# Kernel optimization log

Measured on AMD Instinct MI355X. Metric: run time of the kernel, lower is better.

The kernel has to match this reference:

```python
import jax, jax.numpy as jnp
import numpy as np

SEQ_LEN = 4096
HIDDEN = 1280
NUM_HEADS = 16
HEAD_DIM = HIDDEN // NUM_HEADS  # 80
NUM_SEQS = 8


def setup_inputs() -> dict:
    key = jax.random.key(0)
    ks = jax.random.split(key, 8)
    x = jax.random.normal(ks[0], (SEQ_LEN, HIDDEN), dtype=jnp.float32)
    # rotary tables: use cos/sin of random angles so they are bounded like real RoPE tables
    ang = jax.random.uniform(ks[1], (SEQ_LEN, HEAD_DIM), dtype=jnp.float32) * 6.283185
    cos = jnp.cos(ang)
    sin = jnp.sin(ang)
    # variable-length packed segments: strictly increasing boundaries incl. 0 and SEQ_LEN
    rng = np.random.default_rng(0)
    inner = np.sort(rng.choice(np.arange(1, SEQ_LEN), size=NUM_SEQS - 1, replace=False))
    cu_seqlens = jnp.asarray(np.concatenate([[0], inner, [SEQ_LEN]]), dtype=jnp.int32)
    s = 0.02
    w_qkv = jax.random.normal(ks[2], (HIDDEN, 3 * HIDDEN), dtype=jnp.float32) * s
    b_qkv = jnp.zeros((3 * HIDDEN,), dtype=jnp.float32)
    w_proj = jax.random.normal(ks[3], (HIDDEN, HIDDEN), dtype=jnp.float32) * s
    b_proj = jnp.zeros((HIDDEN,), dtype=jnp.float32)
    return {"x": x, "cu_seqlens": cu_seqlens, "cos": cos, "sin": sin,
            "w_qkv": w_qkv, "b_qkv": b_qkv, "w_proj": w_proj, "b_proj": b_proj}


def _rotate_half(t):
    d = t.shape[-1] // 2
    return jnp.concatenate([-t[..., d:], t[..., :d]], axis=-1)


def _apply_rope(q, k, cos, sin):
    # q,k: (S,H,D); cos,sin: (S,D) broadcast over heads, computed in fp32
    c = cos[:, None, :].astype(jnp.float32)
    s = sin[:, None, :].astype(jnp.float32)
    qf, kf = q.astype(jnp.float32), k.astype(jnp.float32)
    q_out = qf * c + _rotate_half(qf) * s
    k_out = kf * c + _rotate_half(kf) * s
    return q_out.astype(q.dtype), k_out.astype(k.dtype)


def reference(x, cu_seqlens, cos, sin, w_qkv, b_qkv, w_proj, b_proj):
    S = x.shape[0]
    scale = HEAD_DIM ** (-0.5)
    qkv = (x @ w_qkv + b_qkv).reshape(S, 3, NUM_HEADS, HEAD_DIM)
    q, k, v = qkv[:, 0], qkv[:, 1], qkv[:, 2]  # each (S,H,D)
    q, k = _apply_rope(q, k, cos, sin)
    # block-diagonal varlen attention via segment-id mask (same math as per-chunk softmax)
    pos = jnp.arange(S)
    seg = jnp.searchsorted(cu_seqlens[1:], pos, side='right')  # (S,) segment id
    mask = seg[:, None] == seg[None, :]  # (S,S) block-diagonal
    scores = jnp.einsum('shd,thd->hst', q, k) * scale  # (H,S,S)
    scores = jnp.where(mask[None], scores.astype(jnp.float32), jnp.finfo(jnp.float32).min)
    attn = jax.nn.softmax(scores, axis=-1).astype(q.dtype)
    out = jnp.einsum('hst,thd->shd', attn, v).reshape(S, NUM_HEADS * HEAD_DIM)
    return out @ w_proj + b_proj
```

## Files before the change

### kernel.cpp

```cpp
#include <hip/hip_runtime.h>
#include <cstdint>
#include <cstddef>

typedef __bf16 bf16x8 __attribute__((ext_vector_type(8)));
typedef float f32x4 __attribute__((ext_vector_type(4)));

#define SEQ   4096
#define HID   1280
#define NH    16
#define HD    80

__device__ __forceinline__ unsigned short f2bf(float f) {
  unsigned int u = __float_as_uint(f);
  unsigned int r = u + 0x7FFFu + ((u >> 16) & 1u);
  return (unsigned short)(r >> 16);
}
__device__ __forceinline__ float bf2f(unsigned short h) {
  return __uint_as_float(((unsigned int)h) << 16);
}
__device__ __forceinline__ __bf16 us2bf(unsigned short u) {
  union { unsigned short s; __bf16 b; } c; c.s = u; return c.b;
}
__device__ __forceinline__ void dma16(const void* g, void* l) {
  __builtin_amdgcn_global_load_lds((const __attribute__((address_space(1))) unsigned int*)g,
                                   (__attribute__((address_space(3))) unsigned int*)l, 16, 0, 0);
}

__global__ __launch_bounds__(256) void split_hi_kernel(const float* __restrict__ x,
                                                       unsigned short* __restrict__ hi,
                                                       int n4) {
  int i = blockIdx.x * 256 + threadIdx.x;
  if (i >= n4) return;
  float4 v = *((const float4*)x + i);
  *((ushort4*)hi + i) = make_ushort4(f2bf(v.x), f2bf(v.y), f2bf(v.z), f2bf(v.w));
}

__global__ __launch_bounds__(256) void tsplit_kernel(const float* __restrict__ W,
                                                     unsigned short* __restrict__ Thi,
                                                     unsigned short* __restrict__ Tlo,
                                                     int K, int N) {
  __shared__ float tile[32][33];
  int n0 = blockIdx.x * 32, k0 = blockIdx.y * 32;
  int tx = threadIdx.x & 31, ty = threadIdx.x >> 5;
#pragma unroll
  for (int i = 0; i < 32; i += 8)
    tile[ty + i][tx] = W[(size_t)(k0 + ty + i) * N + n0 + tx];
  __syncthreads();
#pragma unroll
  for (int i = 0; i < 32; i += 8) {
    float v = tile[tx][ty + i];
    size_t idx = (size_t)(n0 + ty + i) * K + (size_t)(k0 + tx);
    unsigned short h = f2bf(v);
    Thi[idx] = h;
    Tlo[idx] = f2bf(v - bf2f(h));
  }
}

__global__ __launch_bounds__(256, 3) void gemm128_x2(
    const unsigned short* __restrict__ A, const unsigned short* __restrict__ Bh,
    const unsigned short* __restrict__ Bl, const float* __restrict__ bias,
    float* __restrict__ out0, float* __restrict__ out1, float* __restrict__ out2,
    int M, int N, int K) {
  __shared__ __align__(16) unsigned short sALL[3 * 8192];

  const int t = threadIdx.x;
  const int lane = t & 63, wave = t >> 6;
  const int c16 = lane & 15, quad = lane >> 4;
  const int bm = blockIdx.y * 128, bn = blockIdx.x * 128;
  const int wr = (wave >> 1) * 64, wc = (wave & 1) * 64;
  const int lrow = lane >> 3;
  const int lswz = (lane & 7) ^ lrow;

  f32x4 acc[4][4];
#pragma unroll
  for (int i = 0; i < 4; ++i)
#pragma unroll
    for (int j = 0; j < 4; ++j) acc[i][j] = (f32x4){0.f, 0.f, 0.f, 0.f};

  const unsigned short* gp[12];
#pragma unroll
  for (int i = 0; i < 12; ++i) {
    const int ua = wave * 12 + i;
    const int arr = ua >> 4, sub = ua & 15;
    const unsigned short* g = (arr == 0) ? A : (arr == 1) ? Bh : Bl;
    const int rowg = ((arr == 0) ? bm : bn) + sub * 8 + lrow;
    gp[i] = g + (size_t)rowg * K + lswz * 8;
  }

  for (int k0 = 0; k0 < K; k0 += 64) {
    __syncthreads();
#pragma unroll
    for (int i = 0; i < 12; ++i)
      dma16(gp[i] + k0, &sALL[(wave * 12 + i) * 512]);
    __syncthreads();
#pragma unroll
    for (int ks = 0; ks < 2; ++ks) {
      bf16x8 a[4], bh[4], bl[4];
#pragma unroll
      for (int mi = 0; mi < 4; ++mi) {
        const int row = wr + mi * 16 + c16;
        const int off = row * 64 + (((ks * 4 + quad) ^ (row & 7)) * 8);
        a[mi] = *(const bf16x8*)&sALL[off];
      }
#pragma unroll
      for (int ni = 0; ni < 4; ++ni) {
        const int row = wc + ni * 16 + c16;
        const int off = row * 64 + (((ks * 4 + quad) ^ (row & 7)) * 8);
        bh[ni] = *(const bf16x8*)&sALL[8192 + off];
        bl[ni] = *(const bf16x8*)&sALL[16384 + off];
      }
#pragma unroll
      for (int mi = 0; mi < 4; ++mi)
#pragma unroll
        for (int ni = 0; ni < 4; ++ni) {
          acc[mi][ni] = __builtin_amdgcn_mfma_f32_16x16x32_bf16(a[mi], bh[ni], acc[mi][ni], 0, 0, 0);
          acc[mi][ni] = __builtin_amdgcn_mfma_f32_16x16x32_bf16(a[mi], bl[ni], acc[mi][ni], 0, 0, 0);
        }
    }
  }
#pragma unroll
  for (int ni = 0; ni < 4; ++ni) {
    int colg = bn + wc + ni * 16 + c16;
    float bv = bias[colg];
    float* op;
    int c = colg;
    if (c < 1280) op = out0;
    else if (c < 2560) { op = out1; c -= 1280; }
    else { op = out2; c -= 2560; }
#pragma unroll
    for (int mi = 0; mi < 4; ++mi)
#pragma unroll
      for (int r = 0; r < 4; ++r) {
        int rowg = bm + wr + mi * 16 + quad * 4 + r;
        op[(size_t)rowg * 1280 + c] = acc[mi][ni][r] + bv;
      }
  }
}

__global__ __launch_bounds__(256) void rope_pack_kernel(
    float* __restrict__ qf, const float* __restrict__ kf,
    const float* __restrict__ cs, const float* __restrict__ sn,
    unsigned short* __restrict__ khi, unsigned short* __restrict__ klo) {
  const int h = blockIdx.y;
  const int s = blockIdx.x * 64 + (threadIdx.x >> 2);
  const int p = threadIdx.x & 3;
  float* qrow = qf + (size_t)s * HID + h * HD;
  const float* krow = kf + (size_t)s * HID + h * HD;
  const float* cr = cs + (size_t)s * HD;
  const float* sr = sn + (size_t)s * HD;
  unsigned short* kh = khi + ((size_t)h * SEQ + s) * HD;
  unsigned short* kl = klo + ((size_t)h * SEQ + s) * HD;
#pragma unroll
  for (int j = 0; j < 10; ++j) {
    int d = 10 * p + j;
    float c0 = cr[d], s0 = sr[d], c1 = cr[d + 40], s1 = sr[d + 40];
    float q0 = qrow[d], q1 = qrow[d + 40];
    qrow[d]      = q0 * c0 - q1 * s0;
    qrow[d + 40] = q1 * c1 + q0 * s1;
    float k0 = krow[d], k1 = krow[d + 40];
    float kn0 = k0 * c0 - k1 * s0;
    float kn1 = k1 * c1 + k0 * s1;
    unsigned short h0 = f2bf(kn0), h1 = f2bf(kn1);
    kh[d] = h0;      kl[d] = f2bf(kn0 - bf2f(h0));
    kh[d + 40] = h1; kl[d + 40] = f2bf(kn1 - bf2f(h1));
  }
}

__global__ __launch_bounds__(256) void vt_pack_kernel(const float* __restrict__ vf,
                                                      unsigned short* __restrict__ vthi,
                                                      unsigned short* __restrict__ vtlo) {
  __shared__ unsigned short sTh[80][72];
  __shared__ unsigned short sTl[80][72];
  const int h = blockIdx.y;
  const int s0 = blockIdx.x * 64;
  const int t = threadIdx.x;
  {
    int row = t >> 2, p = (t & 3) * 20;
    const float* src = vf + (size_t)(s0 + row) * HID + h * HD + p;
#pragma unroll
    for (int i = 0; i < 5; ++i) {
      float4 v = *(const float4*)(src + 4 * i);
      float vv[4] = {v.x, v.y, v.z, v.w};
#pragma unroll
      for (int j = 0; j < 4; ++j) {
        int d = p + 4 * i + j;
        unsigned short hu = f2bf(vv[j]);
        sTh[d][row] = hu;
        sTl[d][row] = f2bf(vv[j] - bf2f(hu));
      }
    }
  }
  __syncthreads();
  if (t < 160) {
    int d = t >> 1, half = (t & 1) * 32;
    size_t base = (size_t)(h * HD + d) * SEQ + s0 + half;
#pragma unroll
    for (int i = 0; i < 8; ++i) {
      *(ushort4*)&vthi[base + 4 * i] = *(ushort4*)&sTh[d][half + 4 * i];
      *(ushort4*)&vtlo[base + 4 * i] = *(ushort4*)&sTl[d][half + 4 * i];
    }
  }
}


#define SMAX(SC, MI, LI, PK, AR, KBLO, KBHI)                                   \
  do {                                                                         \
    float mx = -1e30f;                                                         \
    _Pragma("unroll") for (int nt = 0; nt < 4; ++nt)                           \
        _Pragma("unroll") for (int r = 0; r < 4; ++r) {                        \
      const int kg = ck + nt * 16 + quad * 4 + r;                              \
      const bool ok = (kg >= (KBLO)) && (kg < (KBHI));                         \
      float v = ok ? SC[nt][r] : -1e30f;                                       \
      SC[nt][r] = v;                                                           \
      mx = fmaxf(mx, v);                                                       \
    }                                                                          \
    mx = fmaxf(mx, __shfl_xor(mx, 16));                                        \
    mx = fmaxf(mx, __shfl_xor(mx, 32));                                        \
    const float mnew = fmaxf(MI, mx);                                          \
    const float alpha = __expf(MI - mnew);                                     \
    float ps = 0.f;                                                            \
    _Pragma("unroll") for (int nt = 0; nt < 4; ++nt)                           \
        _Pragma("unroll") for (int r = 0; r < 4; ++r) {                        \
      const float s = SC[nt][r];                                               \
      const float p = (s > -1e29f) ? __expf(s - mnew) : 0.f;                   \
      ps += p;                                                                 \
      const unsigned int pu = __float_as_uint(p);                              \
      const unsigned short ph_ = (unsigned short)(pu >> 16);                   \
      const unsigned short pl_ = f2bf(p - bf2f(ph_));                          \
      PK[nt][r] = (unsigned int)ph_ | ((unsigned int)pl_ << 16);               \
    }                                                                          \
    ps += __shfl_xor(ps, 16);                                                  \
    ps += __shfl_xor(ps, 32);                                                  \
    LI = LI * alpha + ps;                                                      \
    MI = mnew;                                                                 \
    _Pragma("unroll") for (int r = 0; r < 4; ++r)                              \
        AR[r] = __uint_as_float((unsigned)__builtin_amdgcn_ds_bpermute(        \
            (quad * 4 + r) << 2, __float_as_int(alpha)));                      \
  } while (0)

#define BUILD_P(PK, PHU, PLU)                                                  \
  do {                                                                         \
    unsigned int vj[8];                                                        \
    _Pragma("unroll") for (int j = 0; j < 8; ++j) {                            \
      const int addr = (j < 4) ? addrA : addrB;                                \
      const int r = j & 3;                                                     \
      const int v0 = __builtin_amdgcn_ds_bpermute(addr, (int)PK[2 * ks + 0][r]); \
      const int v1 = __builtin_amdgcn_ds_bpermute(addr, (int)PK[2 * ks + 1][r]); \
      vj[j] = (unsigned int)((quad & 2) ? v1 : v0);                            \
    }                                                                          \
    PHU.w[0] = __builtin_amdgcn_perm(vj[1], vj[0], 0x05040100u);               \
    PHU.w[1] = __builtin_amdgcn_perm(vj[3], vj[2], 0x05040100u);               \
    PHU.w[2] = __builtin_amdgcn_perm(vj[5], vj[4], 0x05040100u);               \
    PHU.w[3] = __builtin_amdgcn_perm(vj[7], vj[6], 0x05040100u);               \
    PLU.w[0] = __builtin_amdgcn_perm(vj[1], vj[0], 0x07060302u);               \
    PLU.w[1] = __builtin_amdgcn_perm(vj[3], vj[2], 0x07060302u);               \
    PLU.w[2] = __builtin_amdgcn_perm(vj[5], vj[4], 0x07060302u);               \
    PLU.w[3] = __builtin_amdgcn_perm(vj[7], vj[6], 0x07060302u);               \
  } while (0)

__global__ __launch_bounds__(128, 2) void attn_kernel(
    const float* __restrict__ qf, const unsigned short* __restrict__ khi,
    const unsigned short* __restrict__ klo, const unsigned short* __restrict__ vthi,
    const unsigned short* __restrict__ vtlo, const int* __restrict__ cu,
    unsigned short* __restrict__ ohi) {
  __shared__ __align__(16) unsigned short sKh[5120], sKl[5120];
  __shared__ __align__(16) unsigned short sVh[5120], sVl[5120];

  const int t = threadIdx.x;
  const int lane = t & 63, wave = t >> 6;
  const int c16 = lane & 15, quad = lane >> 4;
  const int lr8 = lane >> 3;
  const int vswz = (lane & 7) ^ lr8;
  const int addrA = ((((2 * quad) & 3) * 16) + c16) << 2;
  const int addrB = ((((2 * quad + 1) & 3) * 16) + c16) << 2;

  const unsigned int u = (blockIdx.x & 7) * 128 + (blockIdx.x >> 3);
  const int h = (int)(u >> 6);
  const int r0 = (int)(u & 63u) * 64;

  int cu_r[9];
#pragma unroll
  for (int i = 0; i < 9; ++i) cu_r[i] = cu[i];

  const int q0 = r0 + wave * 16 + c16;
  const int q1 = q0 + 32;
  int sq0 = 0, sq1 = 0, sg0 = 0, sg1 = 0;
#pragma unroll
  for (int i = 1; i < 8; ++i) {
    sq0 += (q0 >= cu_r[i]) ? 1 : 0;
    sq1 += (q1 >= cu_r[i]) ? 1 : 0;
    sg0 += (r0 >= cu_r[i]) ? 1 : 0;
    sg1 += (r0 + 63 >= cu_r[i]) ? 1 : 0;
  }
  const int kb_lo0 = cu_r[sq0], kb_hi0 = cu_r[sq0 + 1];
  const int kb_lo1 = cu_r[sq1], kb_hi1 = cu_r[sq1 + 1];
  const int ck0 = cu_r[sg0] & ~63;
  const int kend = cu_r[sg1 + 1];
  const int nchunk = (kend - ck0 + 63) >> 6;

  const float qsc = 0.11180339887498949f;
  bf16x8 qh0[3], ql0[3], qh1[3], ql1[3];
  {
    const float* qrowA = qf + (size_t)q0 * HID + h * HD;
    const float* qrowB = qf + (size_t)q1 * HID + h * HD;
#pragma unroll
    for (int ks = 0; ks < 3; ++ks) {
      const int d = ks * 32 + quad * 8;
      bf16x8 hA = {}, lA = {}, hB = {}, lB = {};
      if (d < 80) {
        float4 a0 = *(const float4*)(qrowA + d);
        float4 a1 = *(const float4*)(qrowA + d + 4);
        float4 b0 = *(const float4*)(qrowB + d);
        float4 b1 = *(const float4*)(qrowB + d + 4);
        float va[8] = {a0.x, a0.y, a0.z, a0.w, a1.x, a1.y, a1.z, a1.w};
        float vb[8] = {b0.x, b0.y, b0.z, b0.w, b1.x, b1.y, b1.z, b1.w};
#pragma unroll
        for (int j = 0; j < 8; ++j) {
          float v = va[j] * qsc;
          unsigned short hu = f2bf(v);
          hA[j] = us2bf(hu); lA[j] = us2bf(f2bf(v - bf2f(hu)));
          v = vb[j] * qsc;
          hu = f2bf(v);
          hB[j] = us2bf(hu); lB[j] = us2bf(f2bf(v - bf2f(hu)));
        }
      }
      qh0[ks] = hA; ql0[ks] = lA; qh1[ks] = hB; ql1[ks] = lB;
    }
  }

  f32x4 O0[5], O1[5];
#pragma unroll
  for (int dt = 0; dt < 5; ++dt) {
    O0[dt] = (f32x4){0.f, 0.f, 0.f, 0.f};
    O1[dt] = (f32x4){0.f, 0.f, 0.f, 0.f};
  }
  float m0 = -1e30f, l0v = 0.f, m1 = -1e30f, l1v = 0.f;

  auto STAGE_K = [&](int ck) {
    const unsigned short* gk = (wave & 1) ? klo : khi;
    unsigned short* lk = (wave & 1) ? sKl : sKh;
    const size_t kb = ((size_t)h * SEQ + ck) * 80 + lane * 8;
#pragma unroll
    for (int i2 = 0; i2 < 10; ++i2) dma16(gk + kb + i2 * 512, lk + i2 * 512);
  };
  auto STAGE_V = [&](int ck) {
    const unsigned short* gv = (wave & 1) ? vtlo : vthi;
    unsigned short* lv = (wave & 1) ? sVl : sVh;
#pragma unroll
    for (int i2 = 0; i2 < 10; ++i2)
      dma16(gv + (size_t)(h * HD + 8 * i2 + lr8) * SEQ + ck + vswz * 8, lv + i2 * 512);
  };

  STAGE_K(ck0);
  STAGE_V(ck0);
  __syncthreads();

  for (int ci = 0; ci < nchunk; ++ci) {
    const int ck = ck0 + ci * 64;

    f32x4 sc0[4], sc1[4];
#pragma unroll
    for (int nt = 0; nt < 4; ++nt) {
      sc0[nt] = (f32x4){0.f, 0.f, 0.f, 0.f};
      sc1[nt] = (f32x4){0.f, 0.f, 0.f, 0.f};
    }
    __builtin_amdgcn_s_setprio(1);
#pragma unroll
    for (int nt = 0; nt < 4; ++nt) {
      const int krow = nt * 16 + c16;
#pragma unroll
      for (int ks = 0; ks < 3; ++ks) {
        const int d = ks * 32 + quad * 8;
        bf16x8 kh = {}, kl = {};
        if (d < 80) {
          kh = *(const bf16x8*)&sKh[krow * 80 + d];
          kl = *(const bf16x8*)&sKl[krow * 80 + d];
        }
        sc0[nt] = __builtin_amdgcn_mfma_f32_16x16x32_bf16(kh, qh0[ks], sc0[nt], 0, 0, 0);
        sc0[nt] = __builtin_amdgcn_mfma_f32_16x16x32_bf16(kh, ql0[ks], sc0[nt], 0, 0, 0);
        sc0[nt] = __builtin_amdgcn_mfma_f32_16x16x32_bf16(kl, qh0[ks], sc0[nt], 0, 0, 0);
        sc1[nt] = __builtin_amdgcn_mfma_f32_16x16x32_bf16(kh, qh1[ks], sc1[nt], 0, 0, 0);
        sc1[nt] = __builtin_amdgcn_mfma_f32_16x16x32_bf16(kh, ql1[ks], sc1[nt], 0, 0, 0);
        sc1[nt] = __builtin_amdgcn_mfma_f32_16x16x32_bf16(kl, qh1[ks], sc1[nt], 0, 0, 0);
      }
    }
    __builtin_amdgcn_s_setprio(0);

    unsigned int pk0[4][4], pk1[4][4];
    float aR0[4], aR1[4];
    SMAX(sc0, m0, l0v, pk0, aR0, kb_lo0, kb_hi0);
    SMAX(sc1, m1, l1v, pk1, aR1, kb_lo1, kb_hi1);
#pragma unroll
    for (int dt = 0; dt < 5; ++dt) {
      f32x4 o = O0[dt];
      o[0] *= aR0[0]; o[1] *= aR0[1]; o[2] *= aR0[2]; o[3] *= aR0[3];
      O0[dt] = o;
      o = O1[dt];
      o[0] *= aR1[0]; o[1] *= aR1[1]; o[2] *= aR1[2]; o[3] *= aR1[3];
      O1[dt] = o;
    }

    __syncthreads();
    if (ci + 1 < nchunk) STAGE_K(ck + 64);

#pragma unroll
    for (int ks = 0; ks < 2; ++ks) {
      union { unsigned int w[4]; bf16x8 v; } ph0u, pl0u, ph1u, pl1u;
      BUILD_P(pk0, ph0u, pl0u);
      BUILD_P(pk1, ph1u, pl1u);
      const int g = ks * 4 + quad;
      __builtin_amdgcn_s_setprio(1);
#pragma unroll
      for (int dt = 0; dt < 5; ++dt) {
        const int d = dt * 16 + c16;
        const int off = d * 64 + ((g ^ (d & 7)) * 8);
        bf16x8 vh = *(const bf16x8*)&sVh[off];
        bf16x8 vl = *(const bf16x8*)&sVl[off];
        O0[dt] = __builtin_amdgcn_mfma_f32_16x16x32_bf16(ph0u.v, vh, O0[dt], 0, 0, 0);
        O0[dt] = __builtin_amdgcn_mfma_f32_16x16x32_bf16(ph0u.v, vl, O0[dt], 0, 0, 0);
        O0[dt] = __builtin_amdgcn_mfma_f32_16x16x32_bf16(pl0u.v, vh, O0[dt], 0, 0, 0);
        O1[dt] = __builtin_amdgcn_mfma_f32_16x16x32_bf16(ph1u.v, vh, O1[dt], 0, 0, 0);
        O1[dt] = __builtin_amdgcn_mfma_f32_16x16x32_bf16(ph1u.v, vl, O1[dt], 0, 0, 0);
        O1[dt] = __builtin_amdgcn_mfma_f32_16x16x32_bf16(pl1u.v, vh, O1[dt], 0, 0, 0);
      }
      __builtin_amdgcn_s_setprio(0);
    }

    __syncthreads();
    if (ci + 1 < nchunk) STAGE_V(ck + 64);
  }

  const float inv0 = 1.0f / l0v;
  const float inv1 = 1.0f / l1v;
  float iR0[4], iR1[4];
#pragma unroll
  for (int r = 0; r < 4; ++r) {
    iR0[r] = __uint_as_float((unsigned)__builtin_amdgcn_ds_bpermute(
                 (quad * 4 + r) << 2, __float_as_int(inv0)));
    iR1[r] = __uint_as_float((unsigned)__builtin_amdgcn_ds_bpermute(
                 (quad * 4 + r) << 2, __float_as_int(inv1)));
  }
#pragma unroll
  for (int dt = 0; dt < 5; ++dt)
#pragma unroll
    for (int r = 0; r < 4; ++r) {
      const int row0 = r0 + wave * 16 + quad * 4 + r;
      ohi[(size_t)row0 * HID + h * HD + dt * 16 + c16] = f2bf(O0[dt][r] * iR0[r]);
      ohi[(size_t)(row0 + 32) * HID + h * HD + dt * 16 + c16] = f2bf(O1[dt][r] * iR1[r]);
    }
}

extern "C" void kernel_launch(void* const* d_in, const int* in_sizes, int n_in,
                              void* d_out, int out_size, void* d_ws, size_t ws_size,
                              hipStream_t stream) {
  const float* x      = (const float*)d_in[0];
  const int*   cu     = (const int*)d_in[1];
  const float* cs     = (const float*)d_in[2];
  const float* sn     = (const float*)d_in[3];
  const float* w_qkv  = (const float*)d_in[4];
  const float* b_qkv  = (const float*)d_in[5];
  const float* w_proj = (const float*)d_in[6];
  const float* b_proj = (const float*)d_in[7];
  float* out = (float*)d_out;

  char* ws = (char*)d_ws;
  float*          qf     = (float*)(ws + 0);
  float*          kf     = (float*)(ws + 20971520ULL);
  unsigned short* vthi   = (unsigned short*)(ws + 20971520ULL);
  unsigned short* vtlo   = (unsigned short*)(ws + 31457280ULL);
  float*          vf     = (float*)(ws + 41943040ULL);
  unsigned short* o_hi   = (unsigned short*)(ws + 41943040ULL);
  unsigned short* x_hi   = (unsigned short*)(ws + 62914560ULL);
  unsigned short* khi    = (unsigned short*)(ws + 62914560ULL);
  unsigned short* klo    = (unsigned short*)(ws + 73400320ULL);
  unsigned short* wqt_hi = (unsigned short*)(ws + 83886080ULL);
  unsigned short* wqt_lo = (unsigned short*)(ws + 93716480ULL);
  unsigned short* wpt_hi = (unsigned short*)(ws + 103546880ULL);
  unsigned short* wpt_lo = (unsigned short*)(ws + 106823680ULL);

  split_hi_kernel<<<5120, 256, 0, stream>>>(x, x_hi, 1310720);
  tsplit_kernel<<<dim3(120, 40), 256, 0, stream>>>(w_qkv, wqt_hi, wqt_lo, 1280, 3840);
  tsplit_kernel<<<dim3(40, 40), 256, 0, stream>>>(w_proj, wpt_hi, wpt_lo, 1280, 1280);
  gemm128_x2<<<dim3(30, 32), 256, 0, stream>>>(x_hi, wqt_hi, wqt_lo, b_qkv,
                                               qf, kf, vf, 4096, 3840, 1280);
  rope_pack_kernel<<<dim3(64, 16), 256, 0, stream>>>(qf, kf, cs, sn, khi, klo);
  vt_pack_kernel<<<dim3(64, 16), 256, 0, stream>>>(vf, vthi, vtlo);
  attn_kernel<<<1024, 128, 0, stream>>>(qf, khi, klo, vthi, vtlo, cu, o_hi);
  gemm128_x2<<<dim3(10, 32), 256, 0, stream>>>(o_hi, wpt_hi, wpt_lo, b_proj,
                                               out, nullptr, nullptr, 4096, 1280, 1280);
}
```

Before: 410.2 us.

## Switch attention kernel to 32x32x16 MFMA with transposed score layout

Rewrites the attention inner loop to use 32x32x16 bf16 MFMAs, with each wave owning 32 query rows held as the B operand. Scores come out with keys along the accumulator rows, so the row max and sum need only one cross-half shuffle. Probabilities are packed into P operands with v_cvt_pk_bf16_f32 and a single xor-32 shuffle, replacing the previous ds_bpermute gather. The change also swizzles K staging offsets, drops padded k-steps, and stages the bf16 output through LDS so it can be written back with 16-byte stores. In exchange, the accumulators take more registers and the 80-dim output wastes half of the third 32-wide tile.

```diff
diff --git a/kernel.cpp b/kernel.cpp
--- a/kernel.cpp
+++ b/kernel.cpp
@@ -4,6 +4,8 @@
 
 typedef __bf16 bf16x8 __attribute__((ext_vector_type(8)));
 typedef float f32x4 __attribute__((ext_vector_type(4)));
+typedef float f32x16 __attribute__((ext_vector_type(16)));
+typedef unsigned short u16x8 __attribute__((ext_vector_type(8)));
 
 #define SEQ   4096
 #define HID   1280
@@ -25,6 +27,13 @@
   __builtin_amdgcn_global_load_lds((const __attribute__((address_space(1))) unsigned int*)g,
                                    (__attribute__((address_space(3))) unsigned int*)l, 16, 0, 0);
 }
+__device__ __forceinline__ unsigned int cvtpk(float a, float b) {
+  unsigned int w;
+  asm("v_cvt_pk_bf16_f32 %0, %1, %2" : "=v"(w) : "v"(a), "v"(b));
+  return w;
+}
+__device__ __forceinline__ float lo2f(unsigned int w) { return __uint_as_float(w << 16); }
+__device__ __forceinline__ float hi2f(unsigned int w) { return __uint_as_float(w & 0xffff0000u); }
 
 __global__ __launch_bounds__(256) void split_hi_kernel(const float* __restrict__ x,
                                                        unsigned short* __restrict__ hi,
@@ -203,76 +212,26 @@
 }
 
 
-#define SMAX(SC, MI, LI, PK, AR, KBLO, KBHI)                                   \
-  do {                                                                         \
-    float mx = -1e30f;                                                         \
-    _Pragma("unroll") for (int nt = 0; nt < 4; ++nt)                           \
-        _Pragma("unroll") for (int r = 0; r < 4; ++r) {                        \
-      const int kg = ck + nt * 16 + quad * 4 + r;                              \
-      const bool ok = (kg >= (KBLO)) && (kg < (KBHI));                         \
-      float v = ok ? SC[nt][r] : -1e30f;                                       \
-      SC[nt][r] = v;                                                           \
-      mx = fmaxf(mx, v);                                                       \
-    }                                                                          \
-    mx = fmaxf(mx, __shfl_xor(mx, 16));                                        \
-    mx = fmaxf(mx, __shfl_xor(mx, 32));                                        \
-    const float mnew = fmaxf(MI, mx);                                          \
-    const float alpha = __expf(MI - mnew);                                     \
-    float ps = 0.f;                                                            \
-    _Pragma("unroll") for (int nt = 0; nt < 4; ++nt)                           \
-        _Pragma("unroll") for (int r = 0; r < 4; ++r) {                        \
-      const float s = SC[nt][r];                                               \
-      const float p = (s > -1e29f) ? __expf(s - mnew) : 0.f;                   \
-      ps += p;                                                                 \
-      const unsigned int pu = __float_as_uint(p);                              \
-      const unsigned short ph_ = (unsigned short)(pu >> 16);                   \
-      const unsigned short pl_ = f2bf(p - bf2f(ph_));                          \
-      PK[nt][r] = (unsigned int)ph_ | ((unsigned int)pl_ << 16);               \
-    }                                                                          \
-    ps += __shfl_xor(ps, 16);                                                  \
-    ps += __shfl_xor(ps, 32);                                                  \
-    LI = LI * alpha + ps;                                                      \
-    MI = mnew;                                                                 \
-    _Pragma("unroll") for (int r = 0; r < 4; ++r)                              \
-        AR[r] = __uint_as_float((unsigned)__builtin_amdgcn_ds_bpermute(        \
-            (quad * 4 + r) << 2, __float_as_int(alpha)));                      \
-  } while (0)
-
-#define BUILD_P(PK, PHU, PLU)                                                  \
-  do {                                                                         \
-    unsigned int vj[8];                                                        \
-    _Pragma("unroll") for (int j = 0; j < 8; ++j) {                            \
-      const int addr = (j < 4) ? addrA : addrB;                                \
-      const int r = j & 3;                                                     \
-      const int v0 = __builtin_amdgcn_ds_bpermute(addr, (int)PK[2 * ks + 0][r]); \
-      const int v1 = __builtin_amdgcn_ds_bpermute(addr, (int)PK[2 * ks + 1][r]); \
-      vj[j] = (unsigned int)((quad & 2) ? v1 : v0);                            \
-    }                                                                          \
-    PHU.w[0] = __builtin_amdgcn_perm(vj[1], vj[0], 0x05040100u);               \
-    PHU.w[1] = __builtin_amdgcn_perm(vj[3], vj[2], 0x05040100u);               \
-    PHU.w[2] = __builtin_amdgcn_perm(vj[5], vj[4], 0x05040100u);               \
-    PHU.w[3] = __builtin_amdgcn_perm(vj[7], vj[6], 0x05040100u);               \
-    PLU.w[0] = __builtin_amdgcn_perm(vj[1], vj[0], 0x07060302u);               \
-    PLU.w[1] = __builtin_amdgcn_perm(vj[3], vj[2], 0x07060302u);               \
-    PLU.w[2] = __builtin_amdgcn_perm(vj[5], vj[4], 0x07060302u);               \
-    PLU.w[3] = __builtin_amdgcn_perm(vj[7], vj[6], 0x07060302u);               \
-  } while (0)
+#define MFMA32(A, B, C) __builtin_amdgcn_mfma_f32_32x32x16_bf16(A, B, C, 0, 0, 0)
 
 __global__ __launch_bounds__(128, 2) void attn_kernel(
     const float* __restrict__ qf, const unsigned short* __restrict__ khi,
     const unsigned short* __restrict__ klo, const unsigned short* __restrict__ vthi,
     const unsigned short* __restrict__ vtlo, const int* __restrict__ cu,
     unsigned short* __restrict__ ohi) {
-  __shared__ __align__(16) unsigned short sKh[5120], sKl[5120];
-  __shared__ __align__(16) unsigned short sVh[5120], sVl[5120];
+  __shared__ __align__(16) unsigned short sAll[20480];
+  unsigned short* const sKh = sAll;
+  unsigned short* const sKl = sAll + 5120;
+  unsigned short* const sVh = sAll + 10240;
+  unsigned short* const sVl = sAll + 15360;
 
   const int t = threadIdx.x;
   const int lane = t & 63, wave = t >> 6;
-  const int c16 = lane & 15, quad = lane >> 4;
+  const int ln5 = lane & 31;
+  const int hi  = lane >> 5;
+  const int ln7 = lane & 7;
   const int lr8 = lane >> 3;
   const int vswz = (lane & 7) ^ lr8;
-  const int addrA = ((((2 * quad) & 3) * 16) + c16) << 2;
-  const int addrB = ((((2 * quad + 1) & 3) * 16) + c16) << 2;
 
   const unsigned int u = (blockIdx.x & 7) * 128 + (blockIdx.x >> 3);
   const int h = (int)(u >> 6);
@@ -282,66 +241,67 @@
 #pragma unroll
   for (int i = 0; i < 9; ++i) cu_r[i] = cu[i];
 
-  const int q0 = r0 + wave * 16 + c16;
-  const int q1 = q0 + 32;
-  int sq0 = 0, sq1 = 0, sg0 = 0, sg1 = 0;
+  const int q_my = r0 + wave * 32 + ln5;
+  int sq = 0, sg0 = 0, sg1 = 0;
 #pragma unroll
   for (int i = 1; i < 8; ++i) {
-    sq0 += (q0 >= cu_r[i]) ? 1 : 0;
-    sq1 += (q1 >= cu_r[i]) ? 1 : 0;
-    sg0 += (r0 >= cu_r[i]) ? 1 : 0;
+    sq  += (q_my    >= cu_r[i]) ? 1 : 0;
+    sg0 += (r0      >= cu_r[i]) ? 1 : 0;
     sg1 += (r0 + 63 >= cu_r[i]) ? 1 : 0;
   }
-  const int kb_lo0 = cu_r[sq0], kb_hi0 = cu_r[sq0 + 1];
-  const int kb_lo1 = cu_r[sq1], kb_hi1 = cu_r[sq1 + 1];
+  const int kb_lo = cu_r[sq], kb_hi = cu_r[sq + 1];
   const int ck0 = cu_r[sg0] & ~63;
   const int kend = cu_r[sg1 + 1];
   const int nchunk = (kend - ck0 + 63) >> 6;
 
+  int ccol[5];
+#pragma unroll
+  for (int c = 0; c < 5; ++c)
+    ccol[c] = (c < 4) ? ((((2 * c) + hi) ^ ln7) * 8) : ((8 + hi) * 8);
+
+  int koff[10];
+#pragma unroll
+  for (int i = 0; i < 10; ++i) {
+    const int G = i * 64 + lane;
+    const int key = (G * 205) >> 11;
+    const int p = G - key * 10;
+    const int cl = (p < 8) ? (p ^ (key & 7)) : p;
+    koff[i] = key * 80 + cl * 8;
+  }
+
   const float qsc = 0.11180339887498949f;
-  bf16x8 qh0[3], ql0[3], qh1[3], ql1[3];
+  bf16x8 qh[5], ql[5];
   {
-    const float* qrowA = qf + (size_t)q0 * HID + h * HD;
-    const float* qrowB = qf + (size_t)q1 * HID + h * HD;
-#pragma unroll
-    for (int ks = 0; ks < 3; ++ks) {
-      const int d = ks * 32 + quad * 8;
-      bf16x8 hA = {}, lA = {}, hB = {}, lB = {};
-      if (d < 80) {
-        float4 a0 = *(const float4*)(qrowA + d);
-        float4 a1 = *(const float4*)(qrowA + d + 4);
-        float4 b0 = *(const float4*)(qrowB + d);
-        float4 b1 = *(const float4*)(qrowB + d + 4);
-        float va[8] = {a0.x, a0.y, a0.z, a0.w, a1.x, a1.y, a1.z, a1.w};
-        float vb[8] = {b0.x, b0.y, b0.z, b0.w, b1.x, b1.y, b1.z, b1.w};
-#pragma unroll
-        for (int j = 0; j < 8; ++j) {
-          float v = va[j] * qsc;
-          unsigned short hu = f2bf(v);
-          hA[j] = us2bf(hu); lA[j] = us2bf(f2bf(v - bf2f(hu)));
-          v = vb[j] * qsc;
-          hu = f2bf(v);
-          hB[j] = us2bf(hu); lB[j] = us2bf(f2bf(v - bf2f(hu)));
-        }
+    const float* qrow = qf + (size_t)q_my * HID + h * HD;
+#pragma unroll
+    for (int kt = 0; kt < 5; ++kt) {
+      const int d0 = kt * 16 + hi * 8;
+      float4 a0 = *(const float4*)(qrow + d0);
+      float4 a1 = *(const float4*)(qrow + d0 + 4);
+      float va[8] = {a0.x, a0.y, a0.z, a0.w, a1.x, a1.y, a1.z, a1.w};
+      bf16x8 hf, lf;
+#pragma unroll
+      for (int j = 0; j < 8; ++j) {
+        float v = va[j] * qsc;
+        unsigned short hu = f2bf(v);
+        hf[j] = us2bf(hu);
+        lf[j] = us2bf(f2bf(v - bf2f(hu)));
       }
-      qh0[ks] = hA; ql0[ks] = lA; qh1[ks] = hB; ql1[ks] = lB;
-    }
-  }
-
-  f32x4 O0[5], O1[5];
-#pragma unroll
-  for (int dt = 0; dt < 5; ++dt) {
-    O0[dt] = (f32x4){0.f, 0.f, 0.f, 0.f};
-    O1[dt] = (f32x4){0.f, 0.f, 0.f, 0.f};
-  }
-  float m0 = -1e30f, l0v = 0.f, m1 = -1e30f, l1v = 0.f;
+      qh[kt] = hf; ql[kt] = lf;
+    }
+  }
+
+  f32x16 O0, O1, O2;
+#pragma unroll
+  for (int r = 0; r < 16; ++r) { O0[r] = 0.f; O1[r] = 0.f; O2[r] = 0.f; }
+  float m_i = -1e30f, l_i = 0.f;
 
   auto STAGE_K = [&](int ck) {
     const unsigned short* gk = (wave & 1) ? klo : khi;
     unsigned short* lk = (wave & 1) ? sKl : sKh;
-    const size_t kb = ((size_t)h * SEQ + ck) * 80 + lane * 8;
-#pragma unroll
-    for (int i2 = 0; i2 < 10; ++i2) dma16(gk + kb + i2 * 512, lk + i2 * 512);
+    const unsigned short* gb = gk + ((size_t)h * SEQ + ck) * 80;
+#pragma unroll
+    for (int i2 = 0; i2 < 10; ++i2) dma16(gb + koff[i2], lk + i2 * 512);
   };
   auto STAGE_V = [&](int ck) {
     const unsigned short* gv = (wave & 1) ? vtlo : vthi;
@@ -358,96 +318,133 @@
   for (int ci = 0; ci < nchunk; ++ci) {
     const int ck = ck0 + ci * 64;
 
-    f32x4 sc0[4], sc1[4];
-#pragma unroll
-    for (int nt = 0; nt < 4; ++nt) {
-      sc0[nt] = (f32x4){0.f, 0.f, 0.f, 0.f};
-      sc1[nt] = (f32x4){0.f, 0.f, 0.f, 0.f};
-    }
+    f32x16 sc0, sc1;
+#pragma unroll
+    for (int r = 0; r < 16; ++r) { sc0[r] = 0.f; sc1[r] = 0.f; }
     __builtin_amdgcn_s_setprio(1);
 #pragma unroll
-    for (int nt = 0; nt < 4; ++nt) {
-      const int krow = nt * 16 + c16;
-#pragma unroll
-      for (int ks = 0; ks < 3; ++ks) {
-        const int d = ks * 32 + quad * 8;
-        bf16x8 kh = {}, kl = {};
-        if (d < 80) {
-          kh = *(const bf16x8*)&sKh[krow * 80 + d];
-          kl = *(const bf16x8*)&sKl[krow * 80 + d];
-        }
-        sc0[nt] = __builtin_amdgcn_mfma_f32_16x16x32_bf16(kh, qh0[ks], sc0[nt], 0, 0, 0);
-        sc0[nt] = __builtin_amdgcn_mfma_f32_16x16x32_bf16(kh, ql0[ks], sc0[nt], 0, 0, 0);
-        sc0[nt] = __builtin_amdgcn_mfma_f32_16x16x32_bf16(kl, qh0[ks], sc0[nt], 0, 0, 0);
-        sc1[nt] = __builtin_amdgcn_mfma_f32_16x16x32_bf16(kh, qh1[ks], sc1[nt], 0, 0, 0);
-        sc1[nt] = __builtin_amdgcn_mfma_f32_16x16x32_bf16(kh, ql1[ks], sc1[nt], 0, 0, 0);
-        sc1[nt] = __builtin_amdgcn_mfma_f32_16x16x32_bf16(kl, qh1[ks], sc1[nt], 0, 0, 0);
-      }
+    for (int kd = 0; kd < 5; ++kd) {
+      const int col = ccol[kd];
+      bf16x8 kha = *(const bf16x8*)&sKh[ln5 * 80 + col];
+      bf16x8 kla = *(const bf16x8*)&sKl[ln5 * 80 + col];
+      bf16x8 khb = *(const bf16x8*)&sKh[(32 + ln5) * 80 + col];
+      bf16x8 klb = *(const bf16x8*)&sKl[(32 + ln5) * 80 + col];
+      sc0 = MFMA32(kha, qh[kd], sc0); sc1 = MFMA32(khb, qh[kd], sc1);
+      sc0 = MFMA32(kha, ql[kd], sc0); sc1 = MFMA32(khb, ql[kd], sc1);
+      sc0 = MFMA32(kla, qh[kd], sc0); sc1 = MFMA32(klb, qh[kd], sc1);
     }
     __builtin_amdgcn_s_setprio(0);
 
-    unsigned int pk0[4][4], pk1[4][4];
-    float aR0[4], aR1[4];
-    SMAX(sc0, m0, l0v, pk0, aR0, kb_lo0, kb_hi0);
-    SMAX(sc1, m1, l1v, pk1, aR1, kb_lo1, kb_hi1);
-#pragma unroll
-    for (int dt = 0; dt < 5; ++dt) {
-      f32x4 o = O0[dt];
-      o[0] *= aR0[0]; o[1] *= aR0[1]; o[2] *= aR0[2]; o[3] *= aR0[3];
-      O0[dt] = o;
-      o = O1[dt];
-      o[0] *= aR1[0]; o[1] *= aR1[1]; o[2] *= aR1[2]; o[3] *= aR1[3];
-      O1[dt] = o;
-    }
+    float mx = -1e30f;
+#define MSK(SCV, KT2)                                                          \
+    {                                                                          \
+      const int kb = ck + (KT2) * 32 + 4 * hi;                                 \
+      _Pragma("unroll")                                                        \
+      for (int r = 0; r < 16; ++r) {                                           \
+        const int kg = kb + (r & 3) + 8 * (r >> 2);                            \
+        float v = (kg >= kb_lo && kg < kb_hi) ? SCV[r] : -1e30f;               \
+        SCV[r] = v;                                                            \
+        mx = fmaxf(mx, v);                                                     \
+      }                                                                        \
+    }
+    MSK(sc0, 0)
+    MSK(sc1, 1)
+#undef MSK
+    mx = fmaxf(mx, __shfl_xor(mx, 32));
+    const float mnew = fmaxf(m_i, mx);
+    const float alpha = __expf(m_i - mnew);
+    float ps = 0.f;
+#define EXPP(SCV)                                                              \
+    _Pragma("unroll")                                                          \
+    for (int r = 0; r < 16; ++r) {                                             \
+      const float s = SCV[r];                                                  \
+      const float p = (s > -1e29f) ? __expf(s - mnew) : 0.f;                   \
+      ps += p;                                                                 \
+      SCV[r] = p;                                                              \
+    }
+    EXPP(sc0)
+    EXPP(sc1)
+#undef EXPP
+    ps += __shfl_xor(ps, 32);
+    l_i = l_i * alpha + ps;
+    m_i = mnew;
+#pragma unroll
+    for (int r = 0; r < 16; ++r) { O0[r] *= alpha; O1[r] *= alpha; O2[r] *= alpha; }
 
     __syncthreads();
     if (ci + 1 < nchunk) STAGE_K(ck + 64);
 
-#pragma unroll
-    for (int ks = 0; ks < 2; ++ks) {
-      union { unsigned int w[4]; bf16x8 v; } ph0u, pl0u, ph1u, pl1u;
-      BUILD_P(pk0, ph0u, pl0u);
-      BUILD_P(pk1, ph1u, pl1u);
-      const int g = ks * 4 + quad;
-      __builtin_amdgcn_s_setprio(1);
-#pragma unroll
-      for (int dt = 0; dt < 5; ++dt) {
-        const int d = dt * 16 + c16;
-        const int off = d * 64 + ((g ^ (d & 7)) * 8);
-        bf16x8 vh = *(const bf16x8*)&sVh[off];
-        bf16x8 vl = *(const bf16x8*)&sVl[off];
-        O0[dt] = __builtin_amdgcn_mfma_f32_16x16x32_bf16(ph0u.v, vh, O0[dt], 0, 0, 0);
-        O0[dt] = __builtin_amdgcn_mfma_f32_16x16x32_bf16(ph0u.v, vl, O0[dt], 0, 0, 0);
-        O0[dt] = __builtin_amdgcn_mfma_f32_16x16x32_bf16(pl0u.v, vh, O0[dt], 0, 0, 0);
-        O1[dt] = __builtin_amdgcn_mfma_f32_16x16x32_bf16(ph1u.v, vh, O1[dt], 0, 0, 0);
-        O1[dt] = __builtin_amdgcn_mfma_f32_16x16x32_bf16(ph1u.v, vl, O1[dt], 0, 0, 0);
-        O1[dt] = __builtin_amdgcn_mfma_f32_16x16x32_bf16(pl1u.v, vh, O1[dt], 0, 0, 0);
-      }
-      __builtin_amdgcn_s_setprio(0);
-    }
+    __builtin_amdgcn_s_setprio(1);
+#define PV_STEP(SCV, SUB, KT)                                                  \
+    {                                                                          \
+      unsigned int A1 = cvtpk(SCV[(SUB)*8+0], SCV[(SUB)*8+1]);                 \
+      unsigned int A2 = cvtpk(SCV[(SUB)*8+2], SCV[(SUB)*8+3]);                 \
+      unsigned int B1 = cvtpk(SCV[(SUB)*8+4], SCV[(SUB)*8+5]);                 \
+      unsigned int B2 = cvtpk(SCV[(SUB)*8+6], SCV[(SUB)*8+7]);                 \
+      float e0 = SCV[(SUB)*8+0] - lo2f(A1), e1 = SCV[(SUB)*8+1] - hi2f(A1);    \
+      float e2 = SCV[(SUB)*8+2] - lo2f(A2), e3 = SCV[(SUB)*8+3] - hi2f(A2);    \
+      float e4 = SCV[(SUB)*8+4] - lo2f(B1), e5 = SCV[(SUB)*8+5] - hi2f(B1);    \
+      float e6 = SCV[(SUB)*8+6] - lo2f(B2), e7 = SCV[(SUB)*8+7] - hi2f(B2);    \
+      unsigned int C1 = cvtpk(e0, e1), C2 = cvtpk(e2, e3);                     \
+      unsigned int D1 = cvtpk(e4, e5), D2 = cvtpk(e6, e7);                     \
+      unsigned int T1 = (unsigned int)__shfl_xor((int)(hi ? A1 : B1), 32);     \
+      unsigned int T2 = (unsigned int)__shfl_xor((int)(hi ? A2 : B2), 32);     \
+      unsigned int U1 = (unsigned int)__shfl_xor((int)(hi ? C1 : D1), 32);     \
+      unsigned int U2 = (unsigned int)__shfl_xor((int)(hi ? C2 : D2), 32);     \
+      union { unsigned int w[4]; bf16x8 v; } ph_, pl_;                         \
+      ph_.w[0] = hi ? T1 : A1;  ph_.w[1] = hi ? T2 : A2;                       \
+      ph_.w[2] = hi ? B1 : T1;  ph_.w[3] = hi ? B2 : T2;                       \
+      pl_.w[0] = hi ? U1 : C1;  pl_.w[1] = hi ? U2 : C2;                       \
+      pl_.w[2] = hi ? D1 : U1;  pl_.w[3] = hi ? D2 : U2;                       \
+      const int vc = ccol[KT];                                                 \
+      bf16x8 vh0 = *(const bf16x8*)&sVh[ln5 * 64 + vc];                        \
+      bf16x8 vh1 = *(const bf16x8*)&sVh[(32 + ln5) * 64 + vc];                 \
+      bf16x8 vh2 = *(const bf16x8*)&sVh[(64 + (ln5 & 15)) * 64 + vc];          \
+      bf16x8 vl0 = *(const bf16x8*)&sVl[ln5 * 64 + vc];                        \
+      bf16x8 vl1 = *(const bf16x8*)&sVl[(32 + ln5) * 64 + vc];                 \
+      bf16x8 vl2 = *(const bf16x8*)&sVl[(64 + (ln5 & 15)) * 64 + vc];          \
+      O0 = MFMA32(vh0, ph_.v, O0); O1 = MFMA32(vh1, ph_.v, O1);                \
+      O2 = MFMA32(vh2, ph_.v, O2);                                             \
+      O0 = MFMA32(vl0, ph_.v, O0); O1 = MFMA32(vl1, ph_.v, O1);                \
+      O2 = MFMA32(vl2, ph_.v, O2);                                             \
+      O0 = MFMA32(vh0, pl_.v, O0); O1 = MFMA32(vh1, pl_.v, O1);                \
+      O2 = MFMA32(vh2, pl_.v, O2);                                             \
+    }
+    PV_STEP(sc0, 0, 0)
+    PV_STEP(sc0, 1, 1)
+    PV_STEP(sc1, 0, 2)
+    PV_STEP(sc1, 1, 3)
+#undef PV_STEP
+    __builtin_amdgcn_s_setprio(0);
 
     __syncthreads();
     if (ci + 1 < nchunk) STAGE_V(ck + 64);
   }
 
-  const float inv0 = 1.0f / l0v;
-  const float inv1 = 1.0f / l1v;
-  float iR0[4], iR1[4];
-#pragma unroll
-  for (int r = 0; r < 4; ++r) {
-    iR0[r] = __uint_as_float((unsigned)__builtin_amdgcn_ds_bpermute(
-                 (quad * 4 + r) << 2, __float_as_int(inv0)));
-    iR1[r] = __uint_as_float((unsigned)__builtin_amdgcn_ds_bpermute(
-                 (quad * 4 + r) << 2, __float_as_int(inv1)));
-  }
-#pragma unroll
-  for (int dt = 0; dt < 5; ++dt)
-#pragma unroll
-    for (int r = 0; r < 4; ++r) {
-      const int row0 = r0 + wave * 16 + quad * 4 + r;
-      ohi[(size_t)row0 * HID + h * HD + dt * 16 + c16] = f2bf(O0[dt][r] * iR0[r]);
-      ohi[(size_t)(row0 + 32) * HID + h * HD + dt * 16 + c16] = f2bf(O1[dt][r] * iR1[r]);
-    }
+  const float inv = 1.0f / l_i;
+  unsigned short* tr = sAll + wave * 3072;
+#define WR(OV, DT)                                                             \
+  _Pragma("unroll")                                                            \
+  for (int r = 0; r < 16; r += 2) {                                            \
+    if ((DT) < 2 || r < 8) {                                                   \
+      const int d = (DT) * 32 + (r & 3) + 8 * (r >> 2) + 4 * hi;               \
+      unsigned int w = cvtpk(OV[r] * inv, OV[r + 1] * inv);                    \
+      *(unsigned int*)&tr[ln5 * 96 + d] = w;                                   \
+    }                                                                          \
+  }
+  WR(O0, 0)
+  WR(O1, 1)
+  WR(O2, 2)
+#undef WR
+  __syncthreads();
+  {
+    const int qq = lane >> 1, part = lane & 1;
+    const unsigned short* src = tr + qq * 96 + part * 40;
+    unsigned short* dst = ohi + (size_t)(r0 + wave * 32 + qq) * HID + h * HD + part * 40;
+#pragma unroll
+    for (int i = 0; i < 5; ++i)
+      *(u16x8*)&dst[i * 8] = *(const u16x8*)&src[i * 8];
+  }
 }
 
 extern "C" void kernel_launch(void* const* d_in, const int* in_sizes, int n_in,
```

New measurement: 369.0 us. 1.11x faster.
